# Optimization experiments

Measured on AMD Instinct MI355X. Metric: run time of the kernel, lower is better.

Reference implementation:

```python
import jax, jax.numpy as jnp
import numpy as np

D_MODEL = 2048
N_HEADS = 16
D_HEAD = D_MODEL // N_HEADS  # 128
RANK = 32


def _orthogonal(key, rows, cols, dtype=jnp.float32):
    # mimic torch orthogonal init via QR
    a = jax.random.normal(key, (max(rows, cols), min(rows, cols)), dtype=jnp.float32)
    q, r = jnp.linalg.qr(a)
    q = q * jnp.sign(jnp.diagonal(r))
    if rows < cols:
        q = q.T
    return q.astype(dtype)


def setup_inputs() -> dict:
    key = jax.random.key(0)
    ks = jax.random.split(key, 8)
    B, T = 2, 2048
    x = jax.random.normal(ks[0], (B, T, D_MODEL), dtype=jnp.float32)
    s = 1.0 / np.sqrt(D_MODEL)
    Wq = jax.random.uniform(ks[1], (D_MODEL, D_MODEL), minval=-s, maxval=s, dtype=jnp.float32)
    Wk = jax.random.uniform(ks[2], (D_MODEL, D_MODEL), minval=-s, maxval=s, dtype=jnp.float32)
    Wv = jax.random.uniform(ks[3], (D_MODEL, D_MODEL), minval=-s, maxval=s, dtype=jnp.float32)
    Wo = jax.random.uniform(ks[4], (D_MODEL, D_MODEL), minval=-s, maxval=s, dtype=jnp.float32)
    # vein projector: project d_head -> rank, reconstruct rank -> d_head (orthogonal init)
    Wdown = _orthogonal(ks[5], D_HEAD, RANK)   # [d_head, r]
    Wup = _orthogonal(ks[6], RANK, D_HEAD)     # [r, d_head]
    return {"x": x, "Wq": Wq, "Wk": Wk, "Wv": Wv, "Wo": Wo, "Wdown": Wdown, "Wup": Wup}


def reference(x, Wq, Wk, Wv, Wo, Wdown, Wup):
    B, T, D = x.shape
    H, dh, r = N_HEADS, D_HEAD, RANK
    scale = 1.0 / np.sqrt(r)

    def heads(y):  # [B,T,D] -> [B,H,T,dh]
        return y.reshape(B, T, H, dh).transpose(0, 2, 1, 3)

    q = heads(x @ Wq.T)
    k = heads(x @ Wk.T)
    v = heads(x @ Wv.T)

    # project into vein (rank) space: [B,H,T,r]
    q_r = jnp.einsum('bhtd,dr->bhtr', q, Wdown)
    k_r = jnp.einsum('bhtd,dr->bhtr', k, Wdown)
    v_r = jnp.einsum('bhtd,dr->bhtr', v, Wdown)

    scores = jnp.einsum('bhqr,bhkr->bhqk', q_r, k_r) * scale  # [B,H,T,T]
    attn = jax.nn.softmax(scores, axis=-1)
    y_r = jnp.einsum('bhqk,bhkr->bhqr', attn, v_r)            # [B,H,T,r]
    y = jnp.einsum('bhtr,rd->bhtd', y_r, Wup)                  # reconstruct [B,H,T,dh]
    y = y.transpose(0, 2, 1, 3).reshape(B, T, D)
    out = y @ Wo.T
    return out
```

## Files before the change

### kernel.cpp

```cpp
#include <hip/hip_runtime.h>
#include <cstdint>
#include <cstddef>

typedef __bf16 bf16;
typedef __attribute__((ext_vector_type(8))) __bf16 bf16x8;
typedef __attribute__((ext_vector_type(4))) __bf16 bf16x4;
typedef __attribute__((ext_vector_type(2))) __bf16 bf16x2;
typedef __attribute__((ext_vector_type(4))) float f32x4;
typedef unsigned int u32;

#define D_MODEL 2048
#define QSCALE      0.17677669529663687f
#define QSCALE_L2E  (0.17677669529663687f * 1.4426950408889634f)

__device__ inline void async_load16(const void* gp, void* lp) {
  __builtin_amdgcn_global_load_lds(
      (const __attribute__((address_space(1))) u32*)gp,
      (__attribute__((address_space(3))) u32*)lp, 16, 0, 0);
}

__device__ inline float fast_exp2(float x) {
#if __has_builtin(__builtin_amdgcn_exp2f)
  return __builtin_amdgcn_exp2f(x);
#else
  return __expf(x * 0.6931471805599453f);
#endif
}

__global__ __launch_bounds__(256) void cvt_k(const float* __restrict__ x,
                                             bf16* __restrict__ xb) {
  const int i = (blockIdx.x * 256 + threadIdx.x) * 8;
  float4 a = *(const float4*)(x + i);
  float4 b = *(const float4*)(x + i + 4);
  bf16x8 o;
  o[0] = (bf16)a.x; o[1] = (bf16)a.y; o[2] = (bf16)a.z; o[3] = (bf16)a.w;
  o[4] = (bf16)b.x; o[5] = (bf16)b.y; o[6] = (bf16)b.z; o[7] = (bf16)b.w;
  *(bf16x8*)(xb + i) = o;
}

__global__ __launch_bounds__(256) void fold_qkv_k(
    const float* __restrict__ Wq, const float* __restrict__ Wk,
    const float* __restrict__ Wv, const float* __restrict__ Wdown,
    bf16* __restrict__ EffT) {
  __shared__ float wd[128][32];
  const int t = threadIdx.x;
  for (int i = t; i < 128 * 32; i += 256)
    ((float*)wd)[i] = Wdown[i];
  __syncthreads();
  const int mh = blockIdx.x;
  const float* W = (mh < 16) ? Wq : ((mh < 32) ? Wk : Wv);
  const int hrow = (mh & 15) * 128;
  const int d = blockIdx.y * 128 + (t & 127);
  const int rh = (t >> 7) * 16;
  float acc[16];
#pragma unroll
  for (int j = 0; j < 16; ++j) acc[j] = 0.f;
#pragma unroll 4
  for (int k = 0; k < 128; ++k) {
    float w = W[(size_t)(hrow + k) * D_MODEL + d];
    const float* wr = &wd[k][rh];
#pragma unroll
    for (int j = 0; j < 16; ++j) acc[j] += w * wr[j];
  }
  bf16* outp = EffT + (size_t)(mh * 32 + rh) * D_MODEL + d;
#pragma unroll
  for (int j = 0; j < 16; ++j) outp[(size_t)j * D_MODEL] = (bf16)acc[j];
}

__global__ __launch_bounds__(256) void fold_o_k(
    const bf16* __restrict__ Wob, const float* __restrict__ Wup,
    bf16* __restrict__ WoEffT) {
  __shared__ __align__(16) bf16 As_[128 * 128];
  __shared__ __align__(16) bf16 Bs_[32 * 128];
  const int t = threadIdx.x, wave = t >> 6, lane = t & 63;
  const int quad = lane >> 4, lc = lane & 15;
  const int d0 = blockIdx.x * 128, h = blockIdx.y;
#pragma unroll
  for (int a = 0; a < 8; ++a) {
    int r0 = wave * 32 + a * 4;
    int row = r0 + (lane >> 4);
    int g = (lane & 15) ^ (row & 15);
    async_load16(Wob + (size_t)(d0 + row) * 2048 + h * 128 + g * 8,
                 As_ + r0 * 128);
  }
  {
    int row = t >> 3;
    int c0 = (t & 7) * 2;
    const float* src = Wup + row * 128 + c0 * 8;
    float4 f0 = ((const float4*)src)[0], f1 = ((const float4*)src)[1];
    float4 f2 = ((const float4*)src)[2], f3 = ((const float4*)src)[3];
    bf16x8 b0, b1;
    b0[0] = (bf16)f0.x; b0[1] = (bf16)f0.y; b0[2] = (bf16)f0.z; b0[3] = (bf16)f0.w;
    b0[4] = (bf16)f1.x; b0[5] = (bf16)f1.y; b0[6] = (bf16)f1.z; b0[7] = (bf16)f1.w;
    b1[0] = (bf16)f2.x; b1[1] = (bf16)f2.y; b1[2] = (bf16)f2.z; b1[3] = (bf16)f2.w;
    b1[4] = (bf16)f3.x; b1[5] = (bf16)f3.y; b1[6] = (bf16)f3.z; b1[7] = (bf16)f3.w;
    *(bf16x8*)(Bs_ + row * 128 + ((c0 ^ (row & 15)) * 8)) = b0;
    *(bf16x8*)(Bs_ + row * 128 + (((c0 + 1) ^ (row & 15)) * 8)) = b1;
  }
  __syncthreads();
  f32x4 acc[2][2] = {};
  const int wm = wave * 32;
#pragma unroll
  for (int kc = 0; kc < 4; ++kc) {
    bf16x8 af[2], bfr[2];
#pragma unroll
    for (int mi = 0; mi < 2; ++mi) {
      int m = wm + mi * 16 + lc;
      af[mi] = *(const bf16x8*)(As_ + m * 128 + (((kc * 4 + quad) ^ (m & 15)) * 8));
    }
#pragma unroll
    for (int ni = 0; ni < 2; ++ni) {
      int n = ni * 16 + lc;
      bfr[ni] = *(const bf16x8*)(Bs_ + n * 128 + (((kc * 4 + quad) ^ (n & 15)) * 8));
    }
#pragma unroll
    for (int mi = 0; mi < 2; ++mi)
#pragma unroll
      for (int ni = 0; ni < 2; ++ni)
        acc[mi][ni] = __builtin_amdgcn_mfma_f32_16x16x32_bf16(
            af[mi], bfr[ni], acc[mi][ni], 0, 0, 0);
  }
#pragma unroll
  for (int mi = 0; mi < 2; ++mi)
#pragma unroll
    for (int ni = 0; ni < 2; ++ni)
#pragma unroll
      for (int reg = 0; reg < 4; ++reg)
        WoEffT[(size_t)(d0 + wm + mi * 16 + quad * 4 + reg) * 512 + h * 32 +
               ni * 16 + lc] = (bf16)acc[mi][ni][reg];
}

template <int EPI>
__global__ __launch_bounds__(256) void gemm_bt_k(
    const bf16* __restrict__ A, const bf16* __restrict__ Bt,
    void* __restrict__ Cv, int M, int N, int K) {
  __shared__ __align__(16) bf16 As[2][128 * 64];
  __shared__ __align__(16) bf16 Bs[2][128 * 64];
  const int t = threadIdx.x, wave = t >> 6, lane = t & 63;
  const int quad = lane >> 4, lc = lane & 15;
  const size_t m0 = (size_t)blockIdx.x * 128;
  const size_t n0 = (size_t)blockIdx.y * 128;
  const int wm = (wave >> 1) * 64, wn = (wave & 1) * 64;
  const int sr = lane >> 3, ss = lane & 7;
  const bf16* Aga[4]; const bf16* Bga[4]; int Loff[4];
#pragma unroll
  for (int a = 0; a < 4; ++a) {
    int row = wave * 32 + a * 8 + sr;
    Aga[a] = A + (m0 + row) * (size_t)K + (ss ^ (row & 7)) * 8;
    Bga[a] = Bt + (n0 + row) * (size_t)K + (ss ^ (row & 7)) * 8;
    Loff[a] = (wave * 32 + a * 8) * 64;
  }
  f32x4 acc[4][4] = {};
  const int NIT = K >> 6;
#pragma unroll
  for (int a = 0; a < 4; ++a) {
    async_load16(Aga[a], &As[0][Loff[a]]);
    async_load16(Bga[a], &Bs[0][Loff[a]]);
  }
  __syncthreads();
  for (int it = 0; it < NIT; ++it) {
    const int cur = it & 1;
    if (it + 1 < NIT) {
      const int k0 = (it + 1) * 64;
#pragma unroll
      for (int a = 0; a < 4; ++a) {
        async_load16(Aga[a] + k0, &As[1 - cur][Loff[a]]);
        async_load16(Bga[a] + k0, &Bs[1 - cur][Loff[a]]);
      }
    }
    const bf16* Asb = As[cur];
    const bf16* Bsb = Bs[cur];
#pragma unroll
    for (int kc = 0; kc < 2; ++kc) {
      bf16x8 af[4], bfr[4];
#pragma unroll
      for (int mi = 0; mi < 4; ++mi) {
        int m = wm + mi * 16 + lc;
        af[mi] = *(const bf16x8*)(Asb + m * 64 + (((kc * 4 + quad) ^ (m & 7)) * 8));
      }
#pragma unroll
      for (int ni = 0; ni < 4; ++ni) {
        int n = wn + ni * 16 + lc;
        bfr[ni] = *(const bf16x8*)(Bsb + n * 64 + (((kc * 4 + quad) ^ (n & 7)) * 8));
      }
#pragma unroll
      for (int mi = 0; mi < 4; ++mi)
#pragma unroll
        for (int ni = 0; ni < 4; ++ni)
          acc[mi][ni] = __builtin_amdgcn_mfma_f32_16x16x32_bf16(
              af[mi], bfr[ni], acc[mi][ni], 0, 0, 0);
    }
    __syncthreads();
  }

  if (EPI == 0) {
    float* C = (float*)Cv;
#pragma unroll
    for (int mi = 0; mi < 4; ++mi)
#pragma unroll
      for (int ni = 0; ni < 4; ++ni) {
        size_t row = m0 + wm + mi * 16 + quad * 4;
        size_t col = n0 + wn + ni * 16 + lc;
#pragma unroll
        for (int reg = 0; reg < 4; ++reg)
          C[(row + reg) * (size_t)N + col] = acc[mi][ni][reg];
      }
  } else {
    bf16* C = (bf16*)Cv;
#pragma unroll
    for (int mi = 0; mi < 4; ++mi)
#pragma unroll
      for (int ni = 0; ni < 4; ++ni) {
        int n = (int)n0 + wn + ni * 16 + lc;
        int mat = n >> 9, hh = (n >> 5) & 15, r = n & 31;
        float sc = (mat == 0) ? QSCALE_L2E : 1.0f;
        int trow = (int)m0 + wm + mi * 16 + quad * 4;
        int b = trow >> 11, tl = trow & 2047;
        if (mat == 2) {
          int tile = tl >> 7, kin = tl & 127;
          size_t off = ((size_t)(b * 16 + hh) * 3 + 2) * 65536 +
                       (size_t)tile * 4096 + r * 128 +
                       (((kin >> 3) ^ (r & 15)) << 3) + (kin & 7);
          bf16x4 pk;
#pragma unroll
          for (int reg = 0; reg < 4; ++reg) pk[reg] = (bf16)acc[mi][ni][reg];
          *(bf16x4*)(C + off) = pk;
        } else {
#pragma unroll
          for (int reg = 0; reg < 4; ++reg) {
            size_t off = (((size_t)(b * 16 + hh) * 3 + mat) * 2048 + tl + reg) * 32 + r;
            C[off] = (bf16)(acc[mi][ni][reg] * sc);
          }
        }
      }
  }
}

__global__ __launch_bounds__(256) void attn_k(const bf16* __restrict__ QKVr,
                                              bf16* __restrict__ Yr) {
  const int bh = blockIdx.x, qb = blockIdx.y;
  const size_t base = (size_t)bh * 3 * 2048 * 32;
  const bf16* Q  = QKVr + base;
  const bf16* Kr = Q + 2048 * 32;
  const bf16* Vr = Kr + 2048 * 32;
  __shared__ __align__(16) bf16 Ks[2][128 * 32];
  __shared__ __align__(16) bf16 Vt[2][32 * 128];
  __shared__ __align__(16) bf16 Ps[4 * 32 * 128];
  const int t = threadIdx.x, wave = t >> 6, lane = t & 63;
  const int quad = lane >> 4, lc = lane & 15;
  const int qbase = qb * 128 + wave * 32;
  const bf16x8 qf0 = *(const bf16x8*)(Q + (size_t)(qbase + lc) * 32 + quad * 8);
  const bf16x8 qf1 = *(const bf16x8*)(Q + (size_t)(qbase + 16 + lc) * 32 + quad * 8);
  f32x4 o00 = {}, o01 = {}, o10 = {}, o11 = {};
  f32x4 os0 = {}, os1 = {};
  bf16x8 ones;
#pragma unroll
  for (int j = 0; j < 8; ++j) ones[j] = (bf16)1.0f;
  const int krow = wave * 16 + (lane >> 2);
  const bf16* Kg = Kr + (size_t)krow * 32 + ((lane & 3) ^ ((krow >> 1) & 3)) * 8;
  bf16* pw = Ps + wave * 32 * 128;

  async_load16(Kg, &Ks[0][wave * 16 * 32]);
  async_load16(Kg + (size_t)64 * 32, &Ks[0][(64 + wave * 16) * 32]);
  async_load16(Vr + (wave * 2) * 512 + lane * 8, &Vt[0][(wave * 2) * 512]);
  async_load16(Vr + (wave * 2 + 1) * 512 + lane * 8, &Vt[0][(wave * 2 + 1) * 512]);
  __syncthreads();

  for (int it = 0; it < 16; ++it) {
    const int kt = it * 128, cur = it & 1;
    if (it < 15) {
      async_load16(Kg + (size_t)(kt + 128) * 32, &Ks[1 - cur][wave * 16 * 32]);
      async_load16(Kg + (size_t)(kt + 192) * 32, &Ks[1 - cur][(64 + wave * 16) * 32]);
      const bf16* vg = Vr + (size_t)(it + 1) * 4096;
      async_load16(vg + (wave * 2) * 512 + lane * 8, &Vt[1 - cur][(wave * 2) * 512]);
      async_load16(vg + (wave * 2 + 1) * 512 + lane * 8, &Vt[1 - cur][(wave * 2 + 1) * 512]);
    }
    const bf16* ksb = Ks[cur];
#pragma unroll
    for (int ni = 0; ni < 8; ++ni) {
      int n = ni * 16 + lc;
      bf16x8 kf = *(const bf16x8*)(ksb + n * 32 + ((quad ^ ((n >> 1) & 3)) * 8));
      f32x4 z = {0.f, 0.f, 0.f, 0.f};
      f32x4 s0 = __builtin_amdgcn_mfma_f32_16x16x32_bf16(kf, qf0, z, 0, 0, 0);
      f32x4 s1 = __builtin_amdgcn_mfma_f32_16x16x32_bf16(kf, qf1, z, 0, 0, 0);
      bf16x4 p0, p1;
#pragma unroll
      for (int reg = 0; reg < 4; ++reg) {
        p0[reg] = (bf16)fast_exp2(s0[reg]);
        p1[reg] = (bf16)fast_exp2(s1[reg]);
      }
      int off = (((2 * ni + (quad >> 1)) ^ lc) * 8) + (quad & 1) * 4;
      *(bf16x4*)(pw + lc * 128 + off) = p0;
      *(bf16x4*)(pw + (16 + lc) * 128 + off) = p1;
    }
    const bf16* vtb = Vt[cur];
#pragma unroll
    for (int kc = 0; kc < 4; ++kc) {
      int co = ((kc * 4 + quad) ^ lc) * 8;
      bf16x8 pf0 = *(const bf16x8*)(pw + lc * 128 + co);
      bf16x8 pf1 = *(const bf16x8*)(pw + (16 + lc) * 128 + co);
      bf16x8 v0 = *(const bf16x8*)(vtb + lc * 128 + co);
      bf16x8 v1 = *(const bf16x8*)(vtb + (16 + lc) * 128 + co);
      o00 = __builtin_amdgcn_mfma_f32_16x16x32_bf16(pf0, v0, o00, 0, 0, 0);
      o01 = __builtin_amdgcn_mfma_f32_16x16x32_bf16(pf0, v1, o01, 0, 0, 0);
      o10 = __builtin_amdgcn_mfma_f32_16x16x32_bf16(pf1, v0, o10, 0, 0, 0);
      o11 = __builtin_amdgcn_mfma_f32_16x16x32_bf16(pf1, v1, o11, 0, 0, 0);
      os0 = __builtin_amdgcn_mfma_f32_16x16x32_bf16(pf0, ones, os0, 0, 0, 0);
      os1 = __builtin_amdgcn_mfma_f32_16x16x32_bf16(pf1, ones, os1, 0, 0, 0);
    }
    __syncthreads();
  }
  const int b = bh >> 4, h = bh & 15;
#pragma unroll
  for (int reg = 0; reg < 4; ++reg) {
    float i0 = 1.0f / os0[reg];
    float i1 = 1.0f / os1[reg];
    size_t r0 = (size_t)b * 2048 + qbase + quad * 4 + reg;
    size_t r1 = r0 + 16;
    Yr[r0 * 512 + h * 32 + lc]      = (bf16)(o00[reg] * i0);
    Yr[r0 * 512 + h * 32 + 16 + lc] = (bf16)(o01[reg] * i0);
    Yr[r1 * 512 + h * 32 + lc]      = (bf16)(o10[reg] * i1);
    Yr[r1 * 512 + h * 32 + 16 + lc] = (bf16)(o11[reg] * i1);
  }
}

extern "C" void kernel_launch(void* const* d_in, const int* in_sizes, int n_in,
                              void* d_out, int out_size, void* d_ws, size_t ws_size,
                              hipStream_t stream) {
  const float* x     = (const float*)d_in[0];
  const float* Wq    = (const float*)d_in[1];
  const float* Wk    = (const float*)d_in[2];
  const float* Wv    = (const float*)d_in[3];
  const float* Wo    = (const float*)d_in[4];
  const float* Wdown = (const float*)d_in[5];
  const float* Wup   = (const float*)d_in[6];
  float* out = (float*)d_out;

  char* ws = (char*)d_ws;
  bf16* EffT   = (bf16*)(ws);
  bf16* WoEffT = (bf16*)(ws + 6291456);
  bf16* QKVr   = (bf16*)(ws + 8388608);
  bf16* Wob    = (bf16*)(ws + 8388608);
  bf16* Yrb    = (bf16*)(ws + 20971520);
  bf16* xb     = (bf16*)(ws + 25165824);

  cvt_k<<<dim3(4096), dim3(256), 0, stream>>>(x, xb);
  cvt_k<<<dim3(2048), dim3(256), 0, stream>>>(Wo, Wob);
  fold_qkv_k<<<dim3(48, 16), dim3(256), 0, stream>>>(Wq, Wk, Wv, Wdown, EffT);
  fold_o_k<<<dim3(16, 16), dim3(256), 0, stream>>>(Wob, Wup, WoEffT);
  gemm_bt_k<1><<<dim3(32, 12), dim3(256), 0, stream>>>(xb, EffT, QKVr,
                                                       4096, 1536, 2048);
  attn_k<<<dim3(32, 16), dim3(256), 0, stream>>>(QKVr, Yrb);
  gemm_bt_k<0><<<dim3(32, 16), dim3(256), 0, stream>>>(Yrb, WoEffT, out,
                                                       4096, 2048, 512);
}
```

Before: 248.7 us.

## Split attention over KV halves with combine kernel, smaller QKV GEMM tile

Attention now splits the key range into two halves across a third grid dimension, writing unnormalized fp32 partial outputs and row sums that a new combine kernel adds and normalizes into bf16. This doubles the attention block count and shrinks the per-wave P scratch so more blocks fit per CU. The QKV GEMM gets a 64-row M tile with higher occupancy bounds, giving more blocks for the 4096x1536 problem. The trade-off is an extra kernel launch plus fp32 partial traffic, and workspace regions are reused (Sums over EffT, Opart over xb).

```diff
diff --git a/kernel.cpp b/kernel.cpp
--- a/kernel.cpp
+++ b/kernel.cpp
@@ -130,51 +130,56 @@
                ni * 16 + lc] = (bf16)acc[mi][ni][reg];
 }
 
-template <int EPI>
-__global__ __launch_bounds__(256) void gemm_bt_k(
+template <int EPI, int BM>
+__global__ __launch_bounds__(256, (BM == 64 ? 3 : 2)) void gemm_bt_k(
     const bf16* __restrict__ A, const bf16* __restrict__ Bt,
     void* __restrict__ Cv, int M, int N, int K) {
-  __shared__ __align__(16) bf16 As[2][128 * 64];
+  constexpr int MI = BM / 32;
+  constexpr int AR = BM / 4;
+  __shared__ __align__(16) bf16 As[2][BM * 64];
   __shared__ __align__(16) bf16 Bs[2][128 * 64];
   const int t = threadIdx.x, wave = t >> 6, lane = t & 63;
   const int quad = lane >> 4, lc = lane & 15;
-  const size_t m0 = (size_t)blockIdx.x * 128;
+  const size_t m0 = (size_t)blockIdx.x * BM;
   const size_t n0 = (size_t)blockIdx.y * 128;
-  const int wm = (wave >> 1) * 64, wn = (wave & 1) * 64;
+  const int wm = (wave >> 1) * (MI * 16), wn = (wave & 1) * 64;
   const int sr = lane >> 3, ss = lane & 7;
-  const bf16* Aga[4]; const bf16* Bga[4]; int Loff[4];
+  const bf16* Aga[MI]; const bf16* Bga[4]; int LoffA[MI], LoffB[4];
+#pragma unroll
+  for (int a = 0; a < MI; ++a) {
+    int row = wave * AR + a * 8 + sr;
+    Aga[a] = A + (m0 + row) * (size_t)K + (ss ^ (row & 7)) * 8;
+    LoffA[a] = (wave * AR + a * 8) * 64;
+  }
 #pragma unroll
   for (int a = 0; a < 4; ++a) {
     int row = wave * 32 + a * 8 + sr;
-    Aga[a] = A + (m0 + row) * (size_t)K + (ss ^ (row & 7)) * 8;
     Bga[a] = Bt + (n0 + row) * (size_t)K + (ss ^ (row & 7)) * 8;
-    Loff[a] = (wave * 32 + a * 8) * 64;
-  }
-  f32x4 acc[4][4] = {};
+    LoffB[a] = (wave * 32 + a * 8) * 64;
+  }
+  f32x4 acc[MI][4] = {};
   const int NIT = K >> 6;
 #pragma unroll
-  for (int a = 0; a < 4; ++a) {
-    async_load16(Aga[a], &As[0][Loff[a]]);
-    async_load16(Bga[a], &Bs[0][Loff[a]]);
-  }
+  for (int a = 0; a < MI; ++a) async_load16(Aga[a], &As[0][LoffA[a]]);
+#pragma unroll
+  for (int a = 0; a < 4; ++a) async_load16(Bga[a], &Bs[0][LoffB[a]]);
   __syncthreads();
   for (int it = 0; it < NIT; ++it) {
     const int cur = it & 1;
     if (it + 1 < NIT) {
       const int k0 = (it + 1) * 64;
 #pragma unroll
-      for (int a = 0; a < 4; ++a) {
-        async_load16(Aga[a] + k0, &As[1 - cur][Loff[a]]);
-        async_load16(Bga[a] + k0, &Bs[1 - cur][Loff[a]]);
-      }
+      for (int a = 0; a < MI; ++a) async_load16(Aga[a] + k0, &As[1 - cur][LoffA[a]]);
+#pragma unroll
+      for (int a = 0; a < 4; ++a) async_load16(Bga[a] + k0, &Bs[1 - cur][LoffB[a]]);
     }
     const bf16* Asb = As[cur];
     const bf16* Bsb = Bs[cur];
 #pragma unroll
     for (int kc = 0; kc < 2; ++kc) {
-      bf16x8 af[4], bfr[4];
-#pragma unroll
-      for (int mi = 0; mi < 4; ++mi) {
+      bf16x8 af[MI], bfr[4];
+#pragma unroll
+      for (int mi = 0; mi < MI; ++mi) {
         int m = wm + mi * 16 + lc;
         af[mi] = *(const bf16x8*)(Asb + m * 64 + (((kc * 4 + quad) ^ (m & 7)) * 8));
       }
@@ -184,7 +189,7 @@
         bfr[ni] = *(const bf16x8*)(Bsb + n * 64 + (((kc * 4 + quad) ^ (n & 7)) * 8));
       }
 #pragma unroll
-      for (int mi = 0; mi < 4; ++mi)
+      for (int mi = 0; mi < MI; ++mi)
 #pragma unroll
         for (int ni = 0; ni < 4; ++ni)
           acc[mi][ni] = __builtin_amdgcn_mfma_f32_16x16x32_bf16(
@@ -196,7 +201,7 @@
   if (EPI == 0) {
     float* C = (float*)Cv;
 #pragma unroll
-    for (int mi = 0; mi < 4; ++mi)
+    for (int mi = 0; mi < MI; ++mi)
 #pragma unroll
       for (int ni = 0; ni < 4; ++ni) {
         size_t row = m0 + wm + mi * 16 + quad * 4;
@@ -208,7 +213,7 @@
   } else {
     bf16* C = (bf16*)Cv;
 #pragma unroll
-    for (int mi = 0; mi < 4; ++mi)
+    for (int mi = 0; mi < MI; ++mi)
 #pragma unroll
       for (int ni = 0; ni < 4; ++ni) {
         int n = (int)n0 + wn + ni * 16 + lc;
@@ -236,16 +241,17 @@
   }
 }
 
-__global__ __launch_bounds__(256) void attn_k(const bf16* __restrict__ QKVr,
-                                              bf16* __restrict__ Yr) {
-  const int bh = blockIdx.x, qb = blockIdx.y;
-  const size_t base = (size_t)bh * 3 * 2048 * 32;
-  const bf16* Q  = QKVr + base;
-  const bf16* Kr = Q + 2048 * 32;
-  const bf16* Vr = Kr + 2048 * 32;
+__global__ __launch_bounds__(256, 4) void attn_k(const bf16* __restrict__ QKVr,
+                                                 float* __restrict__ Op,
+                                                 float* __restrict__ Sums) {
+  const int bh = blockIdx.x, qb = blockIdx.y, kvh = blockIdx.z;
+  const size_t base = (size_t)bh * 3 * 65536;
+  const bf16* Q   = QKVr + base;
+  const bf16* Kr  = Q + 65536 + (size_t)kvh * 1024 * 32;
+  const bf16* Vrb = Q + 131072 + (size_t)kvh * 8 * 4096;
   __shared__ __align__(16) bf16 Ks[2][128 * 32];
   __shared__ __align__(16) bf16 Vt[2][32 * 128];
-  __shared__ __align__(16) bf16 Ps[4 * 32 * 128];
+  __shared__ __align__(16) bf16 Ps[4 * 32 * 32];
   const int t = threadIdx.x, wave = t >> 6, lane = t & 63;
   const int quad = lane >> 4, lc = lane & 15;
   const int qbase = qb * 128 + wave * 32;
@@ -258,49 +264,52 @@
   for (int j = 0; j < 8; ++j) ones[j] = (bf16)1.0f;
   const int krow = wave * 16 + (lane >> 2);
   const bf16* Kg = Kr + (size_t)krow * 32 + ((lane & 3) ^ ((krow >> 1) & 3)) * 8;
-  bf16* pw = Ps + wave * 32 * 128;
+  bf16* pw = Ps + wave * 32 * 32;
+  const int psw = (lc & 3) ^ (lc >> 2);
 
   async_load16(Kg, &Ks[0][wave * 16 * 32]);
   async_load16(Kg + (size_t)64 * 32, &Ks[0][(64 + wave * 16) * 32]);
-  async_load16(Vr + (wave * 2) * 512 + lane * 8, &Vt[0][(wave * 2) * 512]);
-  async_load16(Vr + (wave * 2 + 1) * 512 + lane * 8, &Vt[0][(wave * 2 + 1) * 512]);
+  async_load16(Vrb + (wave * 2) * 512 + lane * 8, &Vt[0][(wave * 2) * 512]);
+  async_load16(Vrb + (wave * 2 + 1) * 512 + lane * 8, &Vt[0][(wave * 2 + 1) * 512]);
   __syncthreads();
 
-  for (int it = 0; it < 16; ++it) {
+  for (int it = 0; it < 8; ++it) {
     const int kt = it * 128, cur = it & 1;
-    if (it < 15) {
+    if (it < 7) {
       async_load16(Kg + (size_t)(kt + 128) * 32, &Ks[1 - cur][wave * 16 * 32]);
       async_load16(Kg + (size_t)(kt + 192) * 32, &Ks[1 - cur][(64 + wave * 16) * 32]);
-      const bf16* vg = Vr + (size_t)(it + 1) * 4096;
+      const bf16* vg = Vrb + (size_t)(it + 1) * 4096;
       async_load16(vg + (wave * 2) * 512 + lane * 8, &Vt[1 - cur][(wave * 2) * 512]);
       async_load16(vg + (wave * 2 + 1) * 512 + lane * 8, &Vt[1 - cur][(wave * 2 + 1) * 512]);
     }
     const bf16* ksb = Ks[cur];
-#pragma unroll
-    for (int ni = 0; ni < 8; ++ni) {
-      int n = ni * 16 + lc;
-      bf16x8 kf = *(const bf16x8*)(ksb + n * 32 + ((quad ^ ((n >> 1) & 3)) * 8));
-      f32x4 z = {0.f, 0.f, 0.f, 0.f};
-      f32x4 s0 = __builtin_amdgcn_mfma_f32_16x16x32_bf16(kf, qf0, z, 0, 0, 0);
-      f32x4 s1 = __builtin_amdgcn_mfma_f32_16x16x32_bf16(kf, qf1, z, 0, 0, 0);
-      bf16x4 p0, p1;
-#pragma unroll
-      for (int reg = 0; reg < 4; ++reg) {
-        p0[reg] = (bf16)fast_exp2(s0[reg]);
-        p1[reg] = (bf16)fast_exp2(s1[reg]);
-      }
-      int off = (((2 * ni + (quad >> 1)) ^ lc) * 8) + (quad & 1) * 4;
-      *(bf16x4*)(pw + lc * 128 + off) = p0;
-      *(bf16x4*)(pw + (16 + lc) * 128 + off) = p1;
-    }
     const bf16* vtb = Vt[cur];
 #pragma unroll
-    for (int kc = 0; kc < 4; ++kc) {
-      int co = ((kc * 4 + quad) ^ lc) * 8;
-      bf16x8 pf0 = *(const bf16x8*)(pw + lc * 128 + co);
-      bf16x8 pf1 = *(const bf16x8*)(pw + (16 + lc) * 128 + co);
-      bf16x8 v0 = *(const bf16x8*)(vtb + lc * 128 + co);
-      bf16x8 v1 = *(const bf16x8*)(vtb + (16 + lc) * 128 + co);
+    for (int qtr = 0; qtr < 4; ++qtr) {
+#pragma unroll
+      for (int nii = 0; nii < 2; ++nii) {
+        int ni = qtr * 2 + nii;
+        int n = ni * 16 + lc;
+        bf16x8 kf = *(const bf16x8*)(ksb + n * 32 + ((quad ^ ((n >> 1) & 3)) * 8));
+        f32x4 z = {0.f, 0.f, 0.f, 0.f};
+        f32x4 s0 = __builtin_amdgcn_mfma_f32_16x16x32_bf16(kf, qf0, z, 0, 0, 0);
+        f32x4 s1 = __builtin_amdgcn_mfma_f32_16x16x32_bf16(kf, qf1, z, 0, 0, 0);
+        bf16x4 p0, p1;
+#pragma unroll
+        for (int reg = 0; reg < 4; ++reg) {
+          p0[reg] = (bf16)fast_exp2(s0[reg]);
+          p1[reg] = (bf16)fast_exp2(s1[reg]);
+        }
+        int off = (((2 * nii + (quad >> 1)) ^ psw) * 8) + (quad & 1) * 4;
+        *(bf16x4*)(pw + lc * 32 + off) = p0;
+        *(bf16x4*)(pw + (16 + lc) * 32 + off) = p1;
+      }
+      int co = (quad ^ psw) * 8;
+      bf16x8 pf0 = *(const bf16x8*)(pw + lc * 32 + co);
+      bf16x8 pf1 = *(const bf16x8*)(pw + (16 + lc) * 32 + co);
+      int vo = ((qtr * 4 + quad) ^ lc) * 8;
+      bf16x8 v0 = *(const bf16x8*)(vtb + lc * 128 + vo);
+      bf16x8 v1 = *(const bf16x8*)(vtb + (16 + lc) * 128 + vo);
       o00 = __builtin_amdgcn_mfma_f32_16x16x32_bf16(pf0, v0, o00, 0, 0, 0);
       o01 = __builtin_amdgcn_mfma_f32_16x16x32_bf16(pf0, v1, o01, 0, 0, 0);
       o10 = __builtin_amdgcn_mfma_f32_16x16x32_bf16(pf1, v0, o10, 0, 0, 0);
@@ -311,17 +320,46 @@
     __syncthreads();
   }
   const int b = bh >> 4, h = bh & 15;
+  float* op = Op + (size_t)kvh * 4096 * 512;
 #pragma unroll
   for (int reg = 0; reg < 4; ++reg) {
-    float i0 = 1.0f / os0[reg];
-    float i1 = 1.0f / os1[reg];
     size_t r0 = (size_t)b * 2048 + qbase + quad * 4 + reg;
     size_t r1 = r0 + 16;
-    Yr[r0 * 512 + h * 32 + lc]      = (bf16)(o00[reg] * i0);
-    Yr[r0 * 512 + h * 32 + 16 + lc] = (bf16)(o01[reg] * i0);
-    Yr[r1 * 512 + h * 32 + lc]      = (bf16)(o10[reg] * i1);
-    Yr[r1 * 512 + h * 32 + 16 + lc] = (bf16)(o11[reg] * i1);
-  }
+    op[r0 * 512 + h * 32 + lc]      = o00[reg];
+    op[r0 * 512 + h * 32 + 16 + lc] = o01[reg];
+    op[r1 * 512 + h * 32 + lc]      = o10[reg];
+    op[r1 * 512 + h * 32 + 16 + lc] = o11[reg];
+  }
+  if (lc == 0) {
+    float* sp = Sums + (size_t)kvh * 65536 + (size_t)bh * 2048 + qbase;
+#pragma unroll
+    for (int reg = 0; reg < 4; ++reg) {
+      sp[quad * 4 + reg]      = os0[reg];
+      sp[16 + quad * 4 + reg] = os1[reg];
+    }
+  }
+}
+
+__global__ __launch_bounds__(256) void comb_k(const float* __restrict__ Op,
+                                              const float* __restrict__ Sums,
+                                              bf16* __restrict__ Yr) {
+  const int idx = blockIdx.x * 256 + threadIdx.x;
+  const int row = idx >> 6;
+  const int c8 = (idx & 63) * 8;
+  const int b = row >> 11, tl = row & 2047;
+  const int h = c8 >> 5;
+  const size_t si = (size_t)(b * 16 + h) * 2048 + tl;
+  const float inv = 1.0f / (Sums[si] + Sums[65536 + si]);
+  const float4* p0 = (const float4*)(Op + (size_t)row * 512 + c8);
+  const float4* p1 = (const float4*)(Op + 4096 * 512 + (size_t)row * 512 + c8);
+  float4 a0 = p0[0], a1 = p0[1];
+  float4 b0 = p1[0], b1 = p1[1];
+  bf16x8 o;
+  o[0] = (bf16)((a0.x + b0.x) * inv); o[1] = (bf16)((a0.y + b0.y) * inv);
+  o[2] = (bf16)((a0.z + b0.z) * inv); o[3] = (bf16)((a0.w + b0.w) * inv);
+  o[4] = (bf16)((a1.x + b1.x) * inv); o[5] = (bf16)((a1.y + b1.y) * inv);
+  o[6] = (bf16)((a1.z + b1.z) * inv); o[7] = (bf16)((a1.w + b1.w) * inv);
+  *(bf16x8*)(Yr + (size_t)row * 512 + c8) = o;
 }
 
 extern "C" void kernel_launch(void* const* d_in, const int* in_sizes, int n_in,
@@ -337,20 +375,23 @@
   float* out = (float*)d_out;
 
   char* ws = (char*)d_ws;
-  bf16* EffT   = (bf16*)(ws);
-  bf16* WoEffT = (bf16*)(ws + 6291456);
-  bf16* QKVr   = (bf16*)(ws + 8388608);
-  bf16* Wob    = (bf16*)(ws + 8388608);
-  bf16* Yrb    = (bf16*)(ws + 20971520);
-  bf16* xb     = (bf16*)(ws + 25165824);
+  bf16*  EffT   = (bf16*)(ws);
+  float* Sums   = (float*)(ws);
+  bf16*  WoEffT = (bf16*)(ws + 6291456);
+  bf16*  QKVr   = (bf16*)(ws + 8388608);
+  bf16*  Wob    = (bf16*)(ws + 8388608);
+  bf16*  Yrb    = (bf16*)(ws + 20971520);
+  bf16*  xb     = (bf16*)(ws + 25165824);
+  float* Opart  = (float*)(ws + 25165824);
 
   cvt_k<<<dim3(4096), dim3(256), 0, stream>>>(x, xb);
   cvt_k<<<dim3(2048), dim3(256), 0, stream>>>(Wo, Wob);
   fold_qkv_k<<<dim3(48, 16), dim3(256), 0, stream>>>(Wq, Wk, Wv, Wdown, EffT);
   fold_o_k<<<dim3(16, 16), dim3(256), 0, stream>>>(Wob, Wup, WoEffT);
-  gemm_bt_k<1><<<dim3(32, 12), dim3(256), 0, stream>>>(xb, EffT, QKVr,
-                                                       4096, 1536, 2048);
-  attn_k<<<dim3(32, 16), dim3(256), 0, stream>>>(QKVr, Yrb);
-  gemm_bt_k<0><<<dim3(32, 16), dim3(256), 0, stream>>>(Yrb, WoEffT, out,
-                                                       4096, 2048, 512);
-}
+  gemm_bt_k<1, 64><<<dim3(64, 12), dim3(256), 0, stream>>>(xb, EffT, QKVr,
+                                                           4096, 1536, 2048);
+  attn_k<<<dim3(32, 16, 2), dim3(256), 0, stream>>>(QKVr, Opart, Sums);
+  comb_k<<<dim3(1024), dim3(256), 0, stream>>>(Opart, Sums, Yrb);
+  gemm_bt_k<0, 128><<<dim3(32, 16), dim3(256), 0, stream>>>(Yrb, WoEffT, out,
+                                                            4096, 2048, 512);
+}
```

Measured after the change: 241.1 us. 3.1% less time.
